# Optimization experiments

Measured on AMD Instinct MI355X. Metric: run time of the kernel, lower is better.

## Reference

```python
import jax, jax.numpy as jnp
import numpy as np

N, H, DE, E = 100000, 64, 16, 1600000
COORD_SCALE = 0.1


def _lin_params(key, din, dout):
    kw, kb = jax.random.split(key)
    W = jax.random.normal(kw, (din, dout), dtype=jnp.float32) * 0.02
    b = jax.random.normal(kb, (dout,), dtype=jnp.float32) * 0.02
    return W, b


def setup_inputs() -> dict:
    key = jax.random.key(0)
    ks = jax.random.split(key, 10)
    h = jax.random.normal(ks[0], (N, H), dtype=jnp.float32)
    pos = jax.random.normal(ks[1], (N, 3), dtype=jnp.float32)
    edge_index = jax.random.randint(ks[2], (2, E), 0, N, dtype=jnp.int32)
    edge_attr = jax.random.normal(ks[3], (E, DE), dtype=jnp.float32)
    W_e1, b_e1 = _lin_params(ks[4], 2 * H + 1 + DE, H)
    W_e2, b_e2 = _lin_params(ks[5], H, H)
    W_c1, b_c1 = _lin_params(ks[6], H, H)
    W_c2, b_c2 = _lin_params(ks[7], H, 1)
    W_n, b_n = _lin_params(ks[8], 2 * H, H)
    ln_g = jnp.ones((H,), dtype=jnp.float32)
    ln_b = jnp.zeros((H,), dtype=jnp.float32)
    return dict(h=h, pos=pos, edge_index=edge_index, edge_attr=edge_attr,
                W_e1=W_e1, b_e1=b_e1, W_e2=W_e2, b_e2=b_e2,
                W_c1=W_c1, b_c1=b_c1, W_c2=W_c2, b_c2=b_c2,
                W_n=W_n, b_n=b_n, ln_g=ln_g, ln_b=ln_b)


def reference(h, pos, edge_index, edge_attr,
              W_e1, b_e1, W_e2, b_e2,
              W_c1, b_c1, W_c2, b_c2,
              W_n, b_n, ln_g, ln_b):
    src, dst = edge_index[0], edge_index[1]
    pos_src = pos[src]            # [E,3] gather
    pos_dst = pos[dst]
    diff = pos_dst - pos_src      # [E,3]
    dist2 = jnp.clip(jnp.sum(diff * diff, axis=-1, keepdims=True), 0.0, 1000.0)  # [E,1]
    direction = diff / jnp.sqrt(dist2 + 1e-8)

    # edge MLP: phi_e(h_i, h_j, d2, e_ij)
    edge_input = jnp.concatenate([h[src], h[dst], dist2, edge_attr], axis=-1)  # [E, 2H+1+De]
    m = jax.nn.relu(edge_input @ W_e1 + b_e1)
    m_ij = jax.nn.relu(m @ W_e2 + b_e2)  # [E,H]

    # coord MLP -> scalar coef, tanh * scale
    c = jax.nn.relu(m_ij @ W_c1 + b_c1)
    coord_coef = jnp.tanh(c @ W_c2 + b_c2) * COORD_SCALE  # [E,1]
    trans = direction * coord_coef  # [E,3]

    # scatter-add to dst
    delta_pos = jnp.zeros_like(pos).at[dst].add(trans)
    pos_out = pos + delta_pos

    agg_msg = jnp.zeros_like(h).at[dst].add(m_ij)  # [N,H]

    # node MLP + residual + LayerNorm
    h_update = jax.nn.relu(jnp.concatenate([h, agg_msg], axis=-1) @ W_n + b_n)
    x = h + h_update
    mu = jnp.mean(x, axis=-1, keepdims=True)
    var = jnp.mean((x - mu) ** 2, axis=-1, keepdims=True)
    h_out = (x - mu) / jnp.sqrt(var + 1e-5) * ln_g + ln_b
    return h_out, pos_out
```

## Files before the change

kernel.cpp:

```cpp
#include <hip/hip_runtime.h>

using f32x4  = __attribute__((ext_vector_type(4))) float;
using short8 = __attribute__((ext_vector_type(8))) short;

__device__ inline short f2bf(float x) {
    union { float f; unsigned u; } v; v.f = x;
    unsigned r = v.u + 0x7fffu + ((v.u >> 16) & 1u);
    return (short)(r >> 16);
}

__device__ inline short8 pack8(float4 a, float4 b) {
    short8 r;
    r[0] = f2bf(a.x); r[1] = f2bf(a.y); r[2] = f2bf(a.z); r[3] = f2bf(a.w);
    r[4] = f2bf(b.x); r[5] = f2bf(b.y); r[6] = f2bf(b.z); r[7] = f2bf(b.w);
    return r;
}

__device__ inline void atomic_pk_add_bf16(short* addr, unsigned pk) {
    asm volatile("global_atomic_pk_add_bf16 %0, %1, off"
                 :: "v"(addr), "v"(pk) : "memory");
}

__global__ __launch_bounds__(256) void convert_weights(
    const float* __restrict__ We1, const float* __restrict__ We2,
    const float* __restrict__ Wc1, const float* __restrict__ Wn,
    short* __restrict__ W1T, short* __restrict__ W2T,
    short* __restrict__ Wc1T, short* __restrict__ WnT)
{
    const int i = blockIdx.x * 256 + threadIdx.x;
    if (i < 64 * 160) {
        const int n = i / 160, k = i % 160;
        float v = 0.0f;
        if (k < 128)       v = We1[k * 64 + n];
        else if (k < 144)  v = We1[(129 + k - 128) * 64 + n];
        else if (k == 144) v = We1[128 * 64 + n];
        W1T[i] = f2bf(v);
    }
    if (i < 64 * 128) {
        const int n = i / 128, k = i % 128;
        WnT[i] = f2bf(Wn[k * 64 + n]);
    }
    if (i < 64 * 64) {
        const int n = i / 64, k = i % 64;
        W2T[i]  = f2bf(We2[k * 64 + n]);
        Wc1T[i] = f2bf(Wc1[k * 64 + n]);
    }
}

__global__ __launch_bounds__(256) void convert_h(
    const float* __restrict__ h, short* __restrict__ hb, int n8)
{
    const int i = blockIdx.x * 256 + threadIdx.x;
    if (i < n8) {
        const float4* h4 = reinterpret_cast<const float4*>(h);
        reinterpret_cast<short8*>(hb)[i] = pack8(h4[2 * i], h4[2 * i + 1]);
    }
}

__global__ __launch_bounds__(256) void egnn_edge_mfma(
    const short* __restrict__ hb, const float* __restrict__ pos,
    const int* __restrict__ ei, const float* __restrict__ ea,
    const short* __restrict__ W1T, const short* __restrict__ W2T,
    const short* __restrict__ Wc1T,
    const float* __restrict__ be1, const float* __restrict__ be2,
    const float* __restrict__ bc1, const float* __restrict__ bc2,
    const float* __restrict__ Wc2,
    short* __restrict__ aggb, float* __restrict__ dpos, int E)
{
    __shared__ short As[64][168];
    __shared__ float sdir[3][64];
    __shared__ int   sdst[64];

    const int tid = threadIdx.x;
    const int e0  = blockIdx.x * 64;

    {
        const int el = tid >> 2, part = tid & 3;
        const int e = e0 + el;
        if (e < E) {
            const int src = ei[e];
            const int dst = ei[E + e];
            const int node = (part < 2) ? src : dst;
            const short8* hp = reinterpret_cast<const short8*>(
                hb + (size_t)node * 64 + (part & 1) * 32);
            #pragma unroll
            for (int q = 0; q < 4; ++q)
                *reinterpret_cast<short8*>(&As[el][part * 32 + q * 8]) = hp[q];
            if (part == 0) {
                const float4* eap = reinterpret_cast<const float4*>(ea + (size_t)e * 16);
                #pragma unroll
                for (int q = 0; q < 2; ++q)
                    *reinterpret_cast<short8*>(&As[el][128 + q * 8]) =
                        pack8(eap[2 * q], eap[2 * q + 1]);
            } else if (part == 2) {
                const float dx = pos[3 * dst + 0] - pos[3 * src + 0];
                const float dy = pos[3 * dst + 1] - pos[3 * src + 1];
                const float dz = pos[3 * dst + 2] - pos[3 * src + 2];
                const float d2 = fminf(dx * dx + dy * dy + dz * dz, 1000.0f);
                const float inv = 1.0f / sqrtf(d2 + 1e-8f);
                short8 z0 = {f2bf(d2), 0, 0, 0, 0, 0, 0, 0};
                *reinterpret_cast<short8*>(&As[el][144]) = z0;
                sdir[0][el] = dx * inv;
                sdir[1][el] = dy * inv;
                sdir[2][el] = dz * inv;
                sdst[el] = dst;
            } else if (part == 3) {
                short8 z = {0, 0, 0, 0, 0, 0, 0, 0};
                *reinterpret_cast<short8*>(&As[el][152]) = z;
            }
        }
    }
    __syncthreads();

    const int lane = tid & 63;
    const int wave = tid >> 6;
    const int r16  = lane & 15;
    const int kg   = lane >> 4;
    const int mrow = wave * 16 + r16;

    f32x4 acc1[4];
    #pragma unroll
    for (int nt = 0; nt < 4; ++nt) {
        const float b = be1[r16 + nt * 16];
        acc1[nt] = {b, b, b, b};
    }
    #pragma unroll
    for (int kt = 0; kt < 5; ++kt) {
        short8 a = *reinterpret_cast<const short8*>(&As[mrow][kt * 32 + kg * 8]);
        #pragma unroll
        for (int nt = 0; nt < 4; ++nt) {
            short8 b = *reinterpret_cast<const short8*>(
                &W1T[(r16 + nt * 16) * 160 + kt * 32 + kg * 8]);
            acc1[nt] = __builtin_amdgcn_mfma_f32_16x16x32_bf16(a, b, acc1[nt], 0, 0, 0);
        }
    }
    #pragma unroll
    for (int nt = 0; nt < 4; ++nt)
        #pragma unroll
        for (int rg = 0; rg < 4; ++rg)
            As[wave * 16 + kg * 4 + rg][r16 + nt * 16] = f2bf(fmaxf(acc1[nt][rg], 0.0f));

    f32x4 acc2[4];
    #pragma unroll
    for (int nt = 0; nt < 4; ++nt) {
        const float b = be2[r16 + nt * 16];
        acc2[nt] = {b, b, b, b};
    }
    #pragma unroll
    for (int kt = 0; kt < 2; ++kt) {
        short8 a = *reinterpret_cast<const short8*>(&As[mrow][kt * 32 + kg * 8]);
        #pragma unroll
        for (int nt = 0; nt < 4; ++nt) {
            short8 b = *reinterpret_cast<const short8*>(
                &W2T[(r16 + nt * 16) * 64 + kt * 32 + kg * 8]);
            acc2[nt] = __builtin_amdgcn_mfma_f32_16x16x32_bf16(a, b, acc2[nt], 0, 0, 0);
        }
    }
    #pragma unroll
    for (int nt = 0; nt < 4; ++nt)
        #pragma unroll
        for (int rg = 0; rg < 4; ++rg) {
            const float v = fmaxf(acc2[nt][rg], 0.0f);
            acc2[nt][rg] = v;
            As[wave * 16 + kg * 4 + rg][64 + r16 + nt * 16] = f2bf(v);
        }

    f32x4 acc3[4];
    #pragma unroll
    for (int nt = 0; nt < 4; ++nt) {
        const float b = bc1[r16 + nt * 16];
        acc3[nt] = {b, b, b, b};
    }
    #pragma unroll
    for (int kt = 0; kt < 2; ++kt) {
        short8 a = *reinterpret_cast<const short8*>(&As[mrow][64 + kt * 32 + kg * 8]);
        #pragma unroll
        for (int nt = 0; nt < 4; ++nt) {
            short8 b = *reinterpret_cast<const short8*>(
                &Wc1T[(r16 + nt * 16) * 64 + kt * 32 + kg * 8]);
            acc3[nt] = __builtin_amdgcn_mfma_f32_16x16x32_bf16(a, b, acc3[nt], 0, 0, 0);
        }
    }

    float prt[4] = {0.0f, 0.0f, 0.0f, 0.0f};
    #pragma unroll
    for (int nt = 0; nt < 4; ++nt) {
        const float wv = Wc2[r16 + nt * 16];
        #pragma unroll
        for (int rg = 0; rg < 4; ++rg)
            prt[rg] += fmaxf(acc3[nt][rg], 0.0f) * wv;
    }
    #pragma unroll
    for (int off = 1; off < 16; off <<= 1)
        #pragma unroll
        for (int rg = 0; rg < 4; ++rg)
            prt[rg] += __shfl_xor(prt[rg], off);
    const float bc2v = bc2[0];

    if (r16 < 3) {
        #pragma unroll
        for (int rg = 0; rg < 4; ++rg) {
            const int er = wave * 16 + kg * 4 + rg;
            if (e0 + er < E) {
                const float coef = tanhf(prt[rg] + bc2v) * 0.1f;
                unsafeAtomicAdd(&dpos[3 * sdst[er] + r16], sdir[r16][er] * coef);
            }
        }
    }
    #pragma unroll
    for (int rg = 0; rg < 4; ++rg) {
        const int er = wave * 16 + kg * 4 + rg;
        if (e0 + er < E) {
            short* arow = aggb + (size_t)sdst[er] * 64;
            #pragma unroll
            for (int nt = 0; nt < 4; ++nt) {
                const float v  = acc2[nt][rg];
                const float vp = __shfl_xor(v, 1);
                if ((r16 & 1) == (nt >> 1)) {
                    const int col0 = (r16 & ~1) + nt * 16;
                    const unsigned blo = (unsigned short)f2bf((r16 & 1) ? vp : v);
                    const unsigned bhi = (unsigned short)f2bf((r16 & 1) ? v : vp);
                    atomic_pk_add_bf16(arow + col0, blo | (bhi << 16));
                }
            }
        }
    }
}

__global__ __launch_bounds__(256) void egnn_node_mfma(
    const float* __restrict__ h, const short* __restrict__ hb,
    const short* __restrict__ aggb, const float* __restrict__ pos,
    const float* __restrict__ dpos, const short* __restrict__ WnT,
    const float* __restrict__ bn, const float* __restrict__ lng,
    const float* __restrict__ lnb,
    float* __restrict__ h_out, float* __restrict__ pos_out, int N)
{
    __shared__ short As[64][136];
    const int tid = threadIdx.x;
    const int n0  = blockIdx.x * 64;

    if (tid < 64) {
        const int n = n0 + tid;
        if (n < N) {
            #pragma unroll
            for (int c = 0; c < 3; ++c)
                pos_out[(size_t)3 * n + c] = pos[(size_t)3 * n + c] + dpos[(size_t)3 * n + c];
        }
    }

    {
        const int row = tid >> 2, part = tid & 3;
        const int n = n0 + row;
        if (n < N) {
            const short* sp = (part < 2) ? (hb + (size_t)n * 64 + (part & 1) * 32)
                                         : (aggb + (size_t)n * 64 + (part & 1) * 32);
            #pragma unroll
            for (int q = 0; q < 4; ++q)
                *reinterpret_cast<short8*>(&As[row][part * 32 + q * 8]) =
                    *reinterpret_cast<const short8*>(sp + q * 8);
        }
    }
    __syncthreads();

    const int lane = tid & 63;
    const int wave = tid >> 6;
    const int r16  = lane & 15;
    const int kg   = lane >> 4;
    const int mrow = wave * 16 + r16;

    f32x4 acc[4];
    #pragma unroll
    for (int nt = 0; nt < 4; ++nt) {
        const float b = bn[r16 + nt * 16];
        acc[nt] = {b, b, b, b};
    }
    #pragma unroll
    for (int kt = 0; kt < 4; ++kt) {
        short8 a = *reinterpret_cast<const short8*>(&As[mrow][kt * 32 + kg * 8]);
        #pragma unroll
        for (int nt = 0; nt < 4; ++nt) {
            short8 b = *reinterpret_cast<const short8*>(
                &WnT[(r16 + nt * 16) * 128 + kt * 32 + kg * 8]);
            acc[nt] = __builtin_amdgcn_mfma_f32_16x16x32_bf16(a, b, acc[nt], 0, 0, 0);
        }
    }

    float xv[4][4];
    #pragma unroll
    for (int rg = 0; rg < 4; ++rg) {
        const int n = n0 + wave * 16 + kg * 4 + rg;
        const bool ok = n < N;
        #pragma unroll
        for (int nt = 0; nt < 4; ++nt)
            xv[nt][rg] = (ok ? h[(size_t)n * 64 + r16 + nt * 16] : 0.0f)
                         + fmaxf(acc[nt][rg], 0.0f);
    }

    float g[4], bb[4];
    #pragma unroll
    for (int nt = 0; nt < 4; ++nt) { g[nt] = lng[r16 + nt * 16]; bb[nt] = lnb[r16 + nt * 16]; }

    #pragma unroll
    for (int rg = 0; rg < 4; ++rg) {
        float s = xv[0][rg] + xv[1][rg] + xv[2][rg] + xv[3][rg];
        #pragma unroll
        for (int off = 1; off < 16; off <<= 1) s += __shfl_xor(s, off);
        const float mu = s * 0.015625f;
        float q = 0.0f;
        #pragma unroll
        for (int nt = 0; nt < 4; ++nt) { const float d = xv[nt][rg] - mu; q += d * d; }
        #pragma unroll
        for (int off = 1; off < 16; off <<= 1) q += __shfl_xor(q, off);
        const float inv = rsqrtf(q * 0.015625f + 1e-5f);
        const int n = n0 + wave * 16 + kg * 4 + rg;
        if (n < N) {
            #pragma unroll
            for (int nt = 0; nt < 4; ++nt)
                h_out[(size_t)n * 64 + r16 + nt * 16] =
                    (xv[nt][rg] - mu) * inv * g[nt] + bb[nt];
        }
    }
}

extern "C" void kernel_launch(void* const* d_in, const int* in_sizes, int n_in,
                              void* d_out, int out_size, void* d_ws, size_t ws_size,
                              hipStream_t stream)
{
    const float* h   = (const float*)d_in[0];
    const float* pos = (const float*)d_in[1];
    const int*   ei  = (const int*)d_in[2];
    const float* ea  = (const float*)d_in[3];
    const float* We1 = (const float*)d_in[4];
    const float* be1 = (const float*)d_in[5];
    const float* We2 = (const float*)d_in[6];
    const float* be2 = (const float*)d_in[7];
    const float* Wc1 = (const float*)d_in[8];
    const float* bc1 = (const float*)d_in[9];
    const float* Wc2 = (const float*)d_in[10];
    const float* bc2 = (const float*)d_in[11];
    const float* Wn  = (const float*)d_in[12];
    const float* bn  = (const float*)d_in[13];
    const float* lng = (const float*)d_in[14];
    const float* lnb = (const float*)d_in[15];

    const int N = in_sizes[0] / 64;
    const int E = in_sizes[2] / 2;

    short* aggb = (short*)d_ws;
    float* dpos = (float*)(aggb + (size_t)N * 64);
    short* W1T  = (short*)(dpos + (size_t)N * 3);
    short* W2T  = W1T + 64 * 160;
    short* Wc1T = W2T + 64 * 64;
    short* WnT  = Wc1T + 64 * 64;
    short* hbuf = WnT + 64 * 128;

    hipMemsetAsync(d_ws, 0, (size_t)N * 140, stream);
    convert_weights<<<40, 256, 0, stream>>>(We1, We2, Wc1, Wn, W1T, W2T, Wc1T, WnT);
    convert_h<<<(N * 64 / 8 + 255) / 256, 256, 0, stream>>>(h, hbuf, N * 64 / 8);

    float* h_out   = (float*)d_out;
    float* pos_out = h_out + (size_t)N * 64;

    egnn_edge_mfma<<<(E + 63) / 64, 256, 0, stream>>>(
        hbuf, pos, ei, ea, W1T, W2T, Wc1T, be1, be2, bc1, bc2, Wc2, aggb, dpos, E);
    egnn_node_mfma<<<(N + 63) / 64, 256, 0, stream>>>(
        h, hbuf, aggb, pos, dpos, WnT, bn, lng, lnb, h_out, pos_out, N);
}
```

Before: 510.2 us.

## Gather edge operands straight into MFMA registers with per-wave LDS scratch

The edge kernel no longer stages the 64x168 input tile in shared memory behind a block-wide barrier. Each wave now loads its own src/dst node features, edge attributes and distance directly into the MFMA A-operand registers. It uses only a small per-wave 16x72 scratch to re-layout the hidden activations between layers. A launch_bounds occupancy hint of 6 is also added. The aim is to cut LDS traffic, drop the __syncthreads, and raise occupancy so the gathers overlap better. In exchange, each edge's indices and positions are loaded and computed redundantly by four lanes, and the occupancy hint may force register spills.

```diff
diff --git a/kernel.cpp b/kernel.cpp
--- a/kernel.cpp
+++ b/kernel.cpp
@@ -57,7 +57,7 @@
     }
 }
 
-__global__ __launch_bounds__(256) void egnn_edge_mfma(
+__global__ __launch_bounds__(256, 6) void egnn_edge_mfma(
     const short* __restrict__ hb, const float* __restrict__ pos,
     const int* __restrict__ ei, const float* __restrict__ ea,
     const short* __restrict__ W1T, const short* __restrict__ W2T,
@@ -67,56 +67,47 @@
     const float* __restrict__ Wc2,
     short* __restrict__ aggb, float* __restrict__ dpos, int E)
 {
-    __shared__ short As[64][168];
-    __shared__ float sdir[3][64];
-    __shared__ int   sdst[64];
-
-    const int tid = threadIdx.x;
-    const int e0  = blockIdx.x * 64;
-
-    {
-        const int el = tid >> 2, part = tid & 3;
-        const int e = e0 + el;
-        if (e < E) {
-            const int src = ei[e];
-            const int dst = ei[E + e];
-            const int node = (part < 2) ? src : dst;
-            const short8* hp = reinterpret_cast<const short8*>(
-                hb + (size_t)node * 64 + (part & 1) * 32);
-            #pragma unroll
-            for (int q = 0; q < 4; ++q)
-                *reinterpret_cast<short8*>(&As[el][part * 32 + q * 8]) = hp[q];
-            if (part == 0) {
-                const float4* eap = reinterpret_cast<const float4*>(ea + (size_t)e * 16);
-                #pragma unroll
-                for (int q = 0; q < 2; ++q)
-                    *reinterpret_cast<short8*>(&As[el][128 + q * 8]) =
-                        pack8(eap[2 * q], eap[2 * q + 1]);
-            } else if (part == 2) {
-                const float dx = pos[3 * dst + 0] - pos[3 * src + 0];
-                const float dy = pos[3 * dst + 1] - pos[3 * src + 1];
-                const float dz = pos[3 * dst + 2] - pos[3 * src + 2];
-                const float d2 = fminf(dx * dx + dy * dy + dz * dz, 1000.0f);
-                const float inv = 1.0f / sqrtf(d2 + 1e-8f);
-                short8 z0 = {f2bf(d2), 0, 0, 0, 0, 0, 0, 0};
-                *reinterpret_cast<short8*>(&As[el][144]) = z0;
-                sdir[0][el] = dx * inv;
-                sdir[1][el] = dy * inv;
-                sdir[2][el] = dz * inv;
-                sdst[el] = dst;
-            } else if (part == 3) {
-                short8 z = {0, 0, 0, 0, 0, 0, 0, 0};
-                *reinterpret_cast<short8*>(&As[el][152]) = z;
-            }
-        }
-    }
-    __syncthreads();
-
+    __shared__ short M[4][16][72];
+    __shared__ float sdir[4][3][16];
+    __shared__ int   sdst[4][16];
+
+    const int tid  = threadIdx.x;
     const int lane = tid & 63;
     const int wave = tid >> 6;
     const int r16  = lane & 15;
     const int kg   = lane >> 4;
-    const int mrow = wave * 16 + r16;
+    const int eb   = blockIdx.x * 64;
+
+    const int e  = eb + wave * 16 + r16;
+    const int ec = min(e, E - 1);
+    const int src = ei[ec];
+    const int dst = ei[E + ec];
+
+    const float dx = pos[3 * dst + 0] - pos[3 * src + 0];
+    const float dy = pos[3 * dst + 1] - pos[3 * src + 1];
+    const float dz = pos[3 * dst + 2] - pos[3 * src + 2];
+    const float d2 = fminf(dx * dx + dy * dy + dz * dz, 1000.0f);
+    const float inv = 1.0f / sqrtf(d2 + 1e-8f);
+    if (kg == 0) {
+        sdir[wave][0][r16] = dx * inv;
+        sdir[wave][1][r16] = dy * inv;
+        sdir[wave][2][r16] = dz * inv;
+        sdst[wave][r16] = dst;
+    }
+
+    const short8* hs = reinterpret_cast<const short8*>(hb + (size_t)src * 64);
+    const short8* hd = reinterpret_cast<const short8*>(hb + (size_t)dst * 64);
+    const short8 a0 = hs[kg];
+    const short8 a1 = hs[4 + kg];
+    const short8 a2 = hd[kg];
+    const short8 a3 = hd[4 + kg];
+    short8 a4 = {0, 0, 0, 0, 0, 0, 0, 0};
+    if (kg < 2) {
+        const float4* eap = reinterpret_cast<const float4*>(ea + (size_t)ec * 16 + kg * 8);
+        a4 = pack8(eap[0], eap[1]);
+    } else if (kg == 2) {
+        a4[0] = f2bf(d2);
+    }
 
     f32x4 acc1[4];
     #pragma unroll
@@ -125,21 +116,27 @@
         acc1[nt] = {b, b, b, b};
     }
     #pragma unroll
-    for (int kt = 0; kt < 5; ++kt) {
-        short8 a = *reinterpret_cast<const short8*>(&As[mrow][kt * 32 + kg * 8]);
-        #pragma unroll
-        for (int nt = 0; nt < 4; ++nt) {
-            short8 b = *reinterpret_cast<const short8*>(
-                &W1T[(r16 + nt * 16) * 160 + kt * 32 + kg * 8]);
-            acc1[nt] = __builtin_amdgcn_mfma_f32_16x16x32_bf16(a, b, acc1[nt], 0, 0, 0);
-        }
+    for (int nt = 0; nt < 4; ++nt) {
+        const short* wr = W1T + (r16 + nt * 16) * 160 + kg * 8;
+        acc1[nt] = __builtin_amdgcn_mfma_f32_16x16x32_bf16(
+            a0, *reinterpret_cast<const short8*>(wr), acc1[nt], 0, 0, 0);
+        acc1[nt] = __builtin_amdgcn_mfma_f32_16x16x32_bf16(
+            a1, *reinterpret_cast<const short8*>(wr + 32), acc1[nt], 0, 0, 0);
+        acc1[nt] = __builtin_amdgcn_mfma_f32_16x16x32_bf16(
+            a2, *reinterpret_cast<const short8*>(wr + 64), acc1[nt], 0, 0, 0);
+        acc1[nt] = __builtin_amdgcn_mfma_f32_16x16x32_bf16(
+            a3, *reinterpret_cast<const short8*>(wr + 96), acc1[nt], 0, 0, 0);
+        acc1[nt] = __builtin_amdgcn_mfma_f32_16x16x32_bf16(
+            a4, *reinterpret_cast<const short8*>(wr + 128), acc1[nt], 0, 0, 0);
     }
     #pragma unroll
     for (int nt = 0; nt < 4; ++nt)
         #pragma unroll
         for (int rg = 0; rg < 4; ++rg)
-            As[wave * 16 + kg * 4 + rg][r16 + nt * 16] = f2bf(fmaxf(acc1[nt][rg], 0.0f));
-
+            M[wave][kg * 4 + rg][r16 + nt * 16] = f2bf(fmaxf(acc1[nt][rg], 0.0f));
+
+    const short8 a5 = *reinterpret_cast<const short8*>(&M[wave][r16][kg * 8]);
+    const short8 a6 = *reinterpret_cast<const short8*>(&M[wave][r16][32 + kg * 8]);
     f32x4 acc2[4];
     #pragma unroll
     for (int nt = 0; nt < 4; ++nt) {
@@ -147,14 +144,12 @@
         acc2[nt] = {b, b, b, b};
     }
     #pragma unroll
-    for (int kt = 0; kt < 2; ++kt) {
-        short8 a = *reinterpret_cast<const short8*>(&As[mrow][kt * 32 + kg * 8]);
-        #pragma unroll
-        for (int nt = 0; nt < 4; ++nt) {
-            short8 b = *reinterpret_cast<const short8*>(
-                &W2T[(r16 + nt * 16) * 64 + kt * 32 + kg * 8]);
-            acc2[nt] = __builtin_amdgcn_mfma_f32_16x16x32_bf16(a, b, acc2[nt], 0, 0, 0);
-        }
+    for (int nt = 0; nt < 4; ++nt) {
+        const short* wr = W2T + (r16 + nt * 16) * 64 + kg * 8;
+        acc2[nt] = __builtin_amdgcn_mfma_f32_16x16x32_bf16(
+            a5, *reinterpret_cast<const short8*>(wr), acc2[nt], 0, 0, 0);
+        acc2[nt] = __builtin_amdgcn_mfma_f32_16x16x32_bf16(
+            a6, *reinterpret_cast<const short8*>(wr + 32), acc2[nt], 0, 0, 0);
     }
     #pragma unroll
     for (int nt = 0; nt < 4; ++nt)
@@ -162,9 +157,11 @@
         for (int rg = 0; rg < 4; ++rg) {
             const float v = fmaxf(acc2[nt][rg], 0.0f);
             acc2[nt][rg] = v;
-            As[wave * 16 + kg * 4 + rg][64 + r16 + nt * 16] = f2bf(v);
-        }
-
+            M[wave][kg * 4 + rg][r16 + nt * 16] = f2bf(v);
+        }
+
+    const short8 a7 = *reinterpret_cast<const short8*>(&M[wave][r16][kg * 8]);
+    const short8 a8 = *reinterpret_cast<const short8*>(&M[wave][r16][32 + kg * 8]);
     f32x4 acc3[4];
     #pragma unroll
     for (int nt = 0; nt < 4; ++nt) {
@@ -172,14 +169,12 @@
         acc3[nt] = {b, b, b, b};
     }
     #pragma unroll
-    for (int kt = 0; kt < 2; ++kt) {
-        short8 a = *reinterpret_cast<const short8*>(&As[mrow][64 + kt * 32 + kg * 8]);
-        #pragma unroll
-        for (int nt = 0; nt < 4; ++nt) {
-            short8 b = *reinterpret_cast<const short8*>(
-                &Wc1T[(r16 + nt * 16) * 64 + kt * 32 + kg * 8]);
-            acc3[nt] = __builtin_amdgcn_mfma_f32_16x16x32_bf16(a, b, acc3[nt], 0, 0, 0);
-        }
+    for (int nt = 0; nt < 4; ++nt) {
+        const short* wr = Wc1T + (r16 + nt * 16) * 64 + kg * 8;
+        acc3[nt] = __builtin_amdgcn_mfma_f32_16x16x32_bf16(
+            a7, *reinterpret_cast<const short8*>(wr), acc3[nt], 0, 0, 0);
+        acc3[nt] = __builtin_amdgcn_mfma_f32_16x16x32_bf16(
+            a8, *reinterpret_cast<const short8*>(wr + 32), acc3[nt], 0, 0, 0);
     }
 
     float prt[4] = {0.0f, 0.0f, 0.0f, 0.0f};
@@ -200,18 +195,19 @@
     if (r16 < 3) {
         #pragma unroll
         for (int rg = 0; rg < 4; ++rg) {
-            const int er = wave * 16 + kg * 4 + rg;
-            if (e0 + er < E) {
+            const int erl = kg * 4 + rg;
+            if (eb + wave * 16 + erl < E) {
                 const float coef = tanhf(prt[rg] + bc2v) * 0.1f;
-                unsafeAtomicAdd(&dpos[3 * sdst[er] + r16], sdir[r16][er] * coef);
+                unsafeAtomicAdd(&dpos[3 * sdst[wave][erl] + r16],
+                                sdir[wave][r16][erl] * coef);
             }
         }
     }
     #pragma unroll
     for (int rg = 0; rg < 4; ++rg) {
-        const int er = wave * 16 + kg * 4 + rg;
-        if (e0 + er < E) {
-            short* arow = aggb + (size_t)sdst[er] * 64;
+        const int erl = kg * 4 + rg;
+        if (eb + wave * 16 + erl < E) {
+            short* arow = aggb + (size_t)sdst[wave][erl] * 64;
             #pragma unroll
             for (int nt = 0; nt < 4; ++nt) {
                 const float v  = acc2[nt][rg];
```

Measured after the change: 614.5 us. 20.4% more time.
